# Optimization experiments

Hardware: AMD Instinct MI355X
Metric: run time of the kernel (lower is better)

## Reference

```python
import jax, jax.numpy as jnp
import numpy as np

N = 50000       # nodes
E = 800000      # edges (avg degree 16)
D = 64          # input_dim
G = 512         # graphs in batch
HID = 64        # hidden_dim


def setup_inputs() -> dict:
    key = jax.random.key(0)
    ks = jax.random.split(key, 8)
    x = jax.random.normal(ks[0], (N, D), dtype=jnp.float32)
    edge_index = jax.random.randint(ks[1], (2, E), 0, N, dtype=jnp.int64)
    batch = jnp.sort(jax.random.randint(ks[2], (N,), 0, G, dtype=jnp.int64))
    # glorot-ish scaled weights
    W1 = jax.random.normal(ks[3], (D, D), dtype=jnp.float32) * (1.0 / np.sqrt(D))
    b1 = jnp.zeros((D,), dtype=jnp.float32)
    W2 = jax.random.normal(ks[4], (D, 2 * D), dtype=jnp.float32) * (1.0 / np.sqrt(D))
    b2 = jnp.zeros((2 * D,), dtype=jnp.float32)
    Wfc = jax.random.normal(ks[5], (2 * D, HID), dtype=jnp.float32) * (1.0 / np.sqrt(2 * D))
    bfc = jnp.zeros((HID,), dtype=jnp.float32)
    return {"x": x, "edge_index": edge_index, "batch": batch,
            "W1": W1, "b1": b1, "W2": W2, "b2": b2, "Wfc": Wfc, "bfc": bfc}


def _gcn_edges(edge_index, n):
    # add self-loops (PyG GCNConv default) and symmetric normalization
    loop = jnp.arange(n, dtype=edge_index.dtype)
    src = jnp.concatenate([edge_index[0], loop])
    dst = jnp.concatenate([edge_index[1], loop])
    deg = jnp.zeros((n,), jnp.float32).at[dst].add(1.0)  # in-degree incl. self-loop
    dinv = jax.lax.rsqrt(deg)                            # deg >= 1 always
    norm = dinv[src] * dinv[dst]                         # [E+N]
    return src, dst, norm


def _gcn_conv(x, src, dst, norm, W, b):
    h = x @ W                                   # transform first (N, out)
    msg = h[src] * norm[:, None]                # gather + scale (E+N, out)
    out = jnp.zeros_like(h).at[dst].add(msg)    # scatter-add at destination
    return out + b


def reference(x, edge_index, batch, W1, b1, W2, b2, Wfc, bfc):
    n = x.shape[0]
    src, dst, norm = _gcn_edges(edge_index, n)
    h = jax.nn.relu(_gcn_conv(x, src, dst, norm, W1, b1))   # [N, D]
    h = _gcn_conv(h, src, dst, norm, W2, b2)                # [N, 2D]
    # global mean pool per graph
    sums = jax.ops.segment_sum(h, batch, num_segments=G)    # [G, 2D]
    cnt = jax.ops.segment_sum(jnp.ones((n,), h.dtype), batch, num_segments=G)
    pooled = sums / jnp.maximum(cnt, 1.0)[:, None]
    # dropout is identity in eval mode
    return pooled @ Wfc + bfc                                # [G, HID]
```

## Files before the change

### kernel.cpp

```cpp
#include <hip/hip_runtime.h>
#include <hip/hip_fp16.h>

#define NN 50000
#define EE 800000
#define DD 64
#define GG 512
#define HIDD 64
#define D2 128
#define NBLK 196

__device__ inline __half2 mk2(float a, float b) {
    __half2 h; h.x = __float2half_rn(a); h.y = __float2half_rn(b); return h;
}

__global__ void k_zero(int* __restrict__ cnt_in, int* __restrict__ part) {
    int i = blockIdx.x * blockDim.x + threadIdx.x;
    if (i < NN) cnt_in[i] = 0;
    if (i < 256) part[i] = 0;
}

__global__ void k_count_rank(const int* __restrict__ dst, int* __restrict__ cnt_in,
                             int* __restrict__ rank) {
    int e = blockIdx.x * blockDim.x + threadIdx.x;
    if (e < EE) rank[e] = atomicAdd(&cnt_in[dst[e]], 1);
}

__global__ void k_partial(const int* __restrict__ cnt_in, int* __restrict__ part) {
    __shared__ int s[256];
    int t = threadIdx.x, i = blockIdx.x * 256 + t;
    s[t] = (i < NN) ? cnt_in[i] : 0;
    __syncthreads();
    for (int off = 128; off > 0; off >>= 1) {
        if (t < off) s[t] += s[t + off];
        __syncthreads();
    }
    if (t == 0) part[blockIdx.x] = s[0];
}

__global__ void k_scanp(int* __restrict__ part) {
    __shared__ int s[256];
    int t = threadIdx.x;
    int v = part[t];
    s[t] = v;
    __syncthreads();
    for (int off = 1; off < 256; off <<= 1) {
        int add = (t >= off) ? s[t - off] : 0;
        __syncthreads();
        s[t] += add;
        __syncthreads();
    }
    part[t] = s[t] - v;
}

__global__ void k_rowptr(const int* __restrict__ cnt_in, const int* __restrict__ part,
                         int* __restrict__ rowptr) {
    __shared__ int s[256];
    int t = threadIdx.x, i = blockIdx.x * 256 + t;
    int v = (i < NN) ? cnt_in[i] : 0;
    s[t] = v;
    __syncthreads();
    for (int off = 1; off < 256; off <<= 1) {
        int add = (t >= off) ? s[t - off] : 0;
        __syncthreads();
        s[t] += add;
        __syncthreads();
    }
    int excl = s[t] - v + part[blockIdx.x];
    if (i <= NN) rowptr[i] = excl;
}

__global__ void k_place(const int* __restrict__ src, const int* __restrict__ dst,
                        const int* __restrict__ rank, const int* __restrict__ rowptr,
                        int* __restrict__ csr) {
    int e = blockIdx.x * blockDim.x + threadIdx.x;
    if (e < EE)
        csr[rowptr[dst[e]] + rank[e]] = src[e];
}

__global__ __launch_bounds__(256) void k_gemm1(const float* __restrict__ x,
        const float* __restrict__ W1, const int* __restrict__ cnt_in,
        __half2* __restrict__ t1h) {
    __shared__ float As[128][68];
    __shared__ float Bs[DD][DD];
    int t = threadIdx.x;
    int row0 = blockIdx.x * 128;
    #pragma unroll
    for (int j = 0; j < 4; ++j) {
        int id = t + j * 256;
        int k = id >> 4, c4 = (id & 15) * 4;
        *(float4*)&Bs[k][c4] = *(const float4*)&W1[k * DD + c4];
    }
    #pragma unroll
    for (int j = 0; j < 8; ++j) {
        int id = t + j * 256;
        int r = id >> 4, k4 = (id & 15) * 4;
        int gr = row0 + r;
        float4 v = make_float4(0.f, 0.f, 0.f, 0.f);
        if (gr < NN) v = *(const float4*)&x[gr * DD + k4];
        *(float4*)&As[r][k4] = v;
    }
    __syncthreads();
    int rbase = (t >> 3) * 4, cbase = (t & 7) * 8;
    float4 cL0 = make_float4(0.f,0.f,0.f,0.f), cH0 = cL0;
    float4 cL1 = cL0, cH1 = cL0, cL2 = cL0, cH2 = cL0, cL3 = cL0, cH3 = cL0;
    #pragma unroll 2
    for (int k = 0; k < DD; ++k) {
        float4 bL = *(const float4*)&Bs[k][cbase];
        float4 bH = *(const float4*)&Bs[k][cbase + 4];
        float a0 = As[rbase + 0][k];
        float a1 = As[rbase + 1][k];
        float a2 = As[rbase + 2][k];
        float a3 = As[rbase + 3][k];
        cL0 += bL * a0;  cH0 += bH * a0;
        cL1 += bL * a1;  cH1 += bH * a1;
        cL2 += bL * a2;  cH2 += bH * a2;
        cL3 += bL * a3;  cH3 += bH * a3;
    }
    int h2base = (t & 7) * 4;
    int gr0 = row0 + rbase;
    #define STORE_T1(idx, CL, CH) \
        if (gr0 + idx < NN) { \
            float d = rsqrtf((float)cnt_in[gr0 + idx] + 1.0f); \
            __half2 p0 = mk2(CL.x * d, CL.y * d), p1 = mk2(CL.z * d, CL.w * d); \
            __half2 p2 = mk2(CH.x * d, CH.y * d), p3 = mk2(CH.z * d, CH.w * d); \
            uint4 pk; pk.x = *(unsigned*)&p0; pk.y = *(unsigned*)&p1; \
            pk.z = *(unsigned*)&p2; pk.w = *(unsigned*)&p3; \
            *(uint4*)(t1h + (size_t)(gr0 + idx) * 32 + h2base) = pk; }
    STORE_T1(0, cL0, cH0)
    STORE_T1(1, cL1, cH1)
    STORE_T1(2, cL2, cH2)
    STORE_T1(3, cL3, cH3)
    #undef STORE_T1
}

__global__ __launch_bounds__(256) void k_agg1(const int* __restrict__ rowptr,
        const int* __restrict__ csr, const __half2* __restrict__ t1h,
        const int* __restrict__ cnt_in, const float* __restrict__ b1,
        __half2* __restrict__ u_h) {
    int gid = blockIdx.x * blockDim.x + threadIdx.x;
    int node = gid >> 5;
    int p = threadIdx.x & 31;
    if (node >= NN) return;
    int beg = rowptr[node], end = rowptr[node + 1];
    float2 A0 = __half22float2(t1h[(size_t)node * 32 + p]);
    float2 A1 = make_float2(0.f, 0.f), A2 = A1, A3 = A1;
    int e = beg;
    for (; e + 4 <= end; e += 4) {
        int s0 = csr[e], s1 = csr[e + 1], s2 = csr[e + 2], s3 = csr[e + 3];
        float2 v0 = __half22float2(t1h[(size_t)s0 * 32 + p]);
        float2 v1 = __half22float2(t1h[(size_t)s1 * 32 + p]);
        float2 v2 = __half22float2(t1h[(size_t)s2 * 32 + p]);
        float2 v3 = __half22float2(t1h[(size_t)s3 * 32 + p]);
        A0.x += v0.x; A0.y += v0.y;
        A1.x += v1.x; A1.y += v1.y;
        A2.x += v2.x; A2.y += v2.y;
        A3.x += v3.x; A3.y += v3.y;
    }
    for (; e < end; ++e) {
        float2 v = __half22float2(t1h[(size_t)csr[e] * 32 + p]);
        A0.x += v.x; A0.y += v.y;
    }
    float sx = (A0.x + A1.x) + (A2.x + A3.x);
    float sy = (A0.y + A1.y) + (A2.y + A3.y);
    float d = rsqrtf((float)cnt_in[node] + 1.0f);
    float2 bb = ((const float2*)b1)[p];
    float h0 = fmaxf(d * sx + bb.x, 0.0f);
    float h1 = fmaxf(d * sy + bb.y, 0.0f);
    u_h[(size_t)node * 32 + p] = mk2(d * h0, d * h1);
}

__global__ __launch_bounds__(256) void k_agg2(const int* __restrict__ rowptr,
        const int* __restrict__ csr, const __half2* __restrict__ u_h,
        const int* __restrict__ cnt_in, float* __restrict__ w) {
    int gid = blockIdx.x * blockDim.x + threadIdx.x;
    int node = gid >> 5;
    int p = threadIdx.x & 31;
    if (node >= NN) return;
    int beg = rowptr[node], end = rowptr[node + 1];
    float2 A0 = __half22float2(u_h[(size_t)node * 32 + p]);
    float2 A1 = make_float2(0.f, 0.f), A2 = A1, A3 = A1;
    int e = beg;
    for (; e + 4 <= end; e += 4) {
        int s0 = csr[e], s1 = csr[e + 1], s2 = csr[e + 2], s3 = csr[e + 3];
        float2 v0 = __half22float2(u_h[(size_t)s0 * 32 + p]);
        float2 v1 = __half22float2(u_h[(size_t)s1 * 32 + p]);
        float2 v2 = __half22float2(u_h[(size_t)s2 * 32 + p]);
        float2 v3 = __half22float2(u_h[(size_t)s3 * 32 + p]);
        A0.x += v0.x; A0.y += v0.y;
        A1.x += v1.x; A1.y += v1.y;
        A2.x += v2.x; A2.y += v2.y;
        A3.x += v3.x; A3.y += v3.y;
    }
    for (; e < end; ++e) {
        float2 v = __half22float2(u_h[(size_t)csr[e] * 32 + p]);
        A0.x += v.x; A0.y += v.y;
    }
    float d = rsqrtf((float)cnt_in[node] + 1.0f);
    float sx = (A0.x + A1.x) + (A2.x + A3.x);
    float sy = (A0.y + A1.y) + (A2.y + A3.y);
    ((float2*)&w[(size_t)node * DD])[p] = make_float2(d * sx, d * sy);
}

__global__ __launch_bounds__(128) void k_pool2(const float* __restrict__ w,
        const int* __restrict__ batch, const float* __restrict__ W2,
        const float* __restrict__ b2, const float* __restrict__ Wfc,
        const float* __restrict__ bfc, float* __restrict__ out) {
    int g = blockIdx.x;
    int t = threadIdx.x;
    int c = t & 63, half = t >> 6;
    int lo = 0, hi = NN;
    while (lo < hi) { int mid = (lo + hi) >> 1; if (batch[mid] < g) lo = mid + 1; else hi = mid; }
    int beg = lo;
    hi = NN;
    while (lo < hi) { int mid = (lo + hi) >> 1; if (batch[mid] < g + 1) lo = mid + 1; else hi = mid; }
    int end = lo;
    int n = end - beg;

    float s = 0.0f;
    for (int i = beg + half; i < end; i += 2)
        s += w[(size_t)i * DD + c];

    __shared__ float sm[128];
    __shared__ float pm[DD];
    __shared__ float tt[D2];
    sm[t] = s;
    __syncthreads();
    if (t < DD) {
        float scale = (n > 0) ? (1.0f / (float)n) : 0.0f;
        pm[t] = (sm[t] + sm[t + 64]) * scale;
    }
    __syncthreads();
    {
        float acc = (n > 0) ? b2[t] : 0.0f;
        #pragma unroll 4
        for (int k = 0; k < DD; ++k)
            acc += pm[k] * W2[k * D2 + t];
        tt[t] = acc;
    }
    __syncthreads();
    if (t < HIDD) {
        float o = bfc[t];
        #pragma unroll 4
        for (int k = 0; k < D2; ++k)
            o += tt[k] * Wfc[k * HIDD + t];
        out[g * HIDD + t] = o;
    }
}

extern "C" void kernel_launch(void* const* d_in, const int* in_sizes, int n_in,
                              void* d_out, int out_size, void* d_ws, size_t ws_size,
                              hipStream_t stream) {
    const float* x     = (const float*)d_in[0];
    const int*   ei    = (const int*)  d_in[1];
    const int*   batch = (const int*)  d_in[2];
    const float* W1    = (const float*)d_in[3];
    const float* b1    = (const float*)d_in[4];
    const float* W2    = (const float*)d_in[5];
    const float* b2    = (const float*)d_in[6];
    const float* Wfc   = (const float*)d_in[7];
    const float* bfc   = (const float*)d_in[8];
    float* out = (float*)d_out;

    const int* src = ei;
    const int* dst = ei + EE;

    char* base = (char*)d_ws;
    __half2* t1h  = (__half2*)base;
    __half2* u_h  = (__half2*)(base + (size_t)NN * 128);
    float*   w    = (float*)(base + (size_t)NN * 512);
    int* iws    = (int*)(base + (size_t)NN * 512 + (size_t)NN * 256);
    int* cnt_in = iws;
    int* rowptr = cnt_in + 50048;
    int* part   = rowptr + 50304;
    int* rank   = part + 256;
    int* csr    = rank + EE;

    k_zero      <<<NBLK, 256, 0, stream>>>(cnt_in, part);
    k_count_rank<<<(EE + 255) / 256, 256, 0, stream>>>(dst, cnt_in, rank);
    k_partial   <<<NBLK, 256, 0, stream>>>(cnt_in, part);
    k_scanp     <<<1, 256, 0, stream>>>(part);
    k_rowptr    <<<NBLK, 256, 0, stream>>>(cnt_in, part, rowptr);
    k_place     <<<(EE + 255) / 256, 256, 0, stream>>>(src, dst, rank, rowptr, csr);
    k_gemm1     <<<(NN + 127) / 128, 256, 0, stream>>>(x, W1, cnt_in, t1h);
    k_agg1      <<<(NN * 32 + 255) / 256, 256, 0, stream>>>(rowptr, csr, t1h, cnt_in, b1, u_h);
    k_agg2      <<<(NN * 32 + 255) / 256, 256, 0, stream>>>(rowptr, csr, u_h, cnt_in, w);
    k_pool2     <<<GG, 128, 0, stream>>>(w, batch, W2, b2, Wfc, bfc, out);
}
```

Baseline: 219.8 us.

## Fuse second aggregation into per-graph pooling and merge scan kernels

The second neighbor aggregation now runs inside the per-graph pooling kernel: each block handles one graph, its warps aggregate that graph's nodes and reduce them in shared memory. This removes the intermediate w buffer write and read and one launch. The three-kernel row-pointer scan is replaced by one kernel where each block recomputes its prefix by summing all preceding counts. That removes launches but adds redundant reads, and the fused pool kernel has less parallelism and can be imbalanced across graphs.

```diff
diff --git a/kernel.cpp b/kernel.cpp
--- a/kernel.cpp
+++ b/kernel.cpp
@@ -13,10 +13,9 @@
     __half2 h; h.x = __float2half_rn(a); h.y = __float2half_rn(b); return h;
 }
 
-__global__ void k_zero(int* __restrict__ cnt_in, int* __restrict__ part) {
+__global__ void k_zero(int* __restrict__ cnt_in) {
     int i = blockIdx.x * blockDim.x + threadIdx.x;
     if (i < NN) cnt_in[i] = 0;
-    if (i < 256) part[i] = 0;
 }
 
 __global__ void k_count_rank(const int* __restrict__ dst, int* __restrict__ cnt_in,
@@ -25,22 +24,24 @@
     if (e < EE) rank[e] = atomicAdd(&cnt_in[dst[e]], 1);
 }
 
-__global__ void k_partial(const int* __restrict__ cnt_in, int* __restrict__ part) {
+__global__ __launch_bounds__(256) void k_scan_rowptr(const int* __restrict__ cnt_in,
+                                                     int* __restrict__ rowptr) {
+    int b = blockIdx.x, t = threadIdx.x;
+    int base = b * 256;
+    int prior = 0;
+    for (int i = t; i < base; i += 256) prior += cnt_in[i];
+    __shared__ int red[256];
+    red[t] = prior;
+    __syncthreads();
+    for (int off = 128; off > 0; off >>= 1) {
+        if (t < off) red[t] += red[t + off];
+        __syncthreads();
+    }
+    int blockPrefix = red[0];
+    __syncthreads();
+    int i = base + t;
+    int v = (i < NN) ? cnt_in[i] : 0;
     __shared__ int s[256];
-    int t = threadIdx.x, i = blockIdx.x * 256 + t;
-    s[t] = (i < NN) ? cnt_in[i] : 0;
-    __syncthreads();
-    for (int off = 128; off > 0; off >>= 1) {
-        if (t < off) s[t] += s[t + off];
-        __syncthreads();
-    }
-    if (t == 0) part[blockIdx.x] = s[0];
-}
-
-__global__ void k_scanp(int* __restrict__ part) {
-    __shared__ int s[256];
-    int t = threadIdx.x;
-    int v = part[t];
     s[t] = v;
     __syncthreads();
     for (int off = 1; off < 256; off <<= 1) {
@@ -49,24 +50,7 @@
         s[t] += add;
         __syncthreads();
     }
-    part[t] = s[t] - v;
-}
-
-__global__ void k_rowptr(const int* __restrict__ cnt_in, const int* __restrict__ part,
-                         int* __restrict__ rowptr) {
-    __shared__ int s[256];
-    int t = threadIdx.x, i = blockIdx.x * 256 + t;
-    int v = (i < NN) ? cnt_in[i] : 0;
-    s[t] = v;
-    __syncthreads();
-    for (int off = 1; off < 256; off <<= 1) {
-        int add = (t >= off) ? s[t - off] : 0;
-        __syncthreads();
-        s[t] += add;
-        __syncthreads();
-    }
-    int excl = s[t] - v + part[blockIdx.x];
-    if (i <= NN) rowptr[i] = excl;
+    if (i <= NN) rowptr[i] = s[t] - v + blockPrefix;
 }
 
 __global__ void k_place(const int* __restrict__ src, const int* __restrict__ dst,
@@ -169,45 +153,15 @@
     u_h[(size_t)node * 32 + p] = mk2(d * h0, d * h1);
 }
 
-__global__ __launch_bounds__(256) void k_agg2(const int* __restrict__ rowptr,
+__global__ __launch_bounds__(256) void k_pool3(const int* __restrict__ rowptr,
         const int* __restrict__ csr, const __half2* __restrict__ u_h,
-        const int* __restrict__ cnt_in, float* __restrict__ w) {
-    int gid = blockIdx.x * blockDim.x + threadIdx.x;
-    int node = gid >> 5;
-    int p = threadIdx.x & 31;
-    if (node >= NN) return;
-    int beg = rowptr[node], end = rowptr[node + 1];
-    float2 A0 = __half22float2(u_h[(size_t)node * 32 + p]);
-    float2 A1 = make_float2(0.f, 0.f), A2 = A1, A3 = A1;
-    int e = beg;
-    for (; e + 4 <= end; e += 4) {
-        int s0 = csr[e], s1 = csr[e + 1], s2 = csr[e + 2], s3 = csr[e + 3];
-        float2 v0 = __half22float2(u_h[(size_t)s0 * 32 + p]);
-        float2 v1 = __half22float2(u_h[(size_t)s1 * 32 + p]);
-        float2 v2 = __half22float2(u_h[(size_t)s2 * 32 + p]);
-        float2 v3 = __half22float2(u_h[(size_t)s3 * 32 + p]);
-        A0.x += v0.x; A0.y += v0.y;
-        A1.x += v1.x; A1.y += v1.y;
-        A2.x += v2.x; A2.y += v2.y;
-        A3.x += v3.x; A3.y += v3.y;
-    }
-    for (; e < end; ++e) {
-        float2 v = __half22float2(u_h[(size_t)csr[e] * 32 + p]);
-        A0.x += v.x; A0.y += v.y;
-    }
-    float d = rsqrtf((float)cnt_in[node] + 1.0f);
-    float sx = (A0.x + A1.x) + (A2.x + A3.x);
-    float sy = (A0.y + A1.y) + (A2.y + A3.y);
-    ((float2*)&w[(size_t)node * DD])[p] = make_float2(d * sx, d * sy);
-}
-
-__global__ __launch_bounds__(128) void k_pool2(const float* __restrict__ w,
-        const int* __restrict__ batch, const float* __restrict__ W2,
-        const float* __restrict__ b2, const float* __restrict__ Wfc,
-        const float* __restrict__ bfc, float* __restrict__ out) {
+        const int* __restrict__ cnt_in, const int* __restrict__ batch,
+        const float* __restrict__ W2, const float* __restrict__ b2,
+        const float* __restrict__ Wfc, const float* __restrict__ bfc,
+        float* __restrict__ out) {
     int g = blockIdx.x;
     int t = threadIdx.x;
-    int c = t & 63, half = t >> 6;
+    int sw = t >> 5, p = t & 31;
     int lo = 0, hi = NN;
     while (lo < hi) { int mid = (lo + hi) >> 1; if (batch[mid] < g) lo = mid + 1; else hi = mid; }
     int beg = lo;
@@ -216,21 +170,46 @@
     int end = lo;
     int n = end - beg;
 
-    float s = 0.0f;
-    for (int i = beg + half; i < end; i += 2)
-        s += w[(size_t)i * DD + c];
-
-    __shared__ float sm[128];
+    float2 gacc = make_float2(0.f, 0.f);
+    for (int node = beg + sw; node < end; node += 8) {
+        int nb = rowptr[node], ne = rowptr[node + 1];
+        float2 A0 = __half22float2(u_h[(size_t)node * 32 + p]);
+        float2 A1 = make_float2(0.f, 0.f), A2 = A1, A3 = A1;
+        int e = nb;
+        for (; e + 4 <= ne; e += 4) {
+            int s0 = csr[e], s1 = csr[e + 1], s2 = csr[e + 2], s3 = csr[e + 3];
+            float2 v0 = __half22float2(u_h[(size_t)s0 * 32 + p]);
+            float2 v1 = __half22float2(u_h[(size_t)s1 * 32 + p]);
+            float2 v2 = __half22float2(u_h[(size_t)s2 * 32 + p]);
+            float2 v3 = __half22float2(u_h[(size_t)s3 * 32 + p]);
+            A0.x += v0.x; A0.y += v0.y;
+            A1.x += v1.x; A1.y += v1.y;
+            A2.x += v2.x; A2.y += v2.y;
+            A3.x += v3.x; A3.y += v3.y;
+        }
+        for (; e < ne; ++e) {
+            float2 v = __half22float2(u_h[(size_t)csr[e] * 32 + p]);
+            A0.x += v.x; A0.y += v.y;
+        }
+        float d = rsqrtf((float)cnt_in[node] + 1.0f);
+        gacc.x += d * ((A0.x + A1.x) + (A2.x + A3.x));
+        gacc.y += d * ((A0.y + A1.y) + (A2.y + A3.y));
+    }
+    __shared__ float2 red[32][9];
+    red[p][sw] = gacc;
+    __syncthreads();
     __shared__ float pm[DD];
+    if (t < 32) {
+        float2 s = red[t][0];
+        #pragma unroll
+        for (int j = 1; j < 8; ++j) { s.x += red[t][j].x; s.y += red[t][j].y; }
+        float scale = (n > 0) ? (1.0f / (float)n) : 0.0f;
+        pm[2 * t]     = s.x * scale;
+        pm[2 * t + 1] = s.y * scale;
+    }
+    __syncthreads();
     __shared__ float tt[D2];
-    sm[t] = s;
-    __syncthreads();
-    if (t < DD) {
-        float scale = (n > 0) ? (1.0f / (float)n) : 0.0f;
-        pm[t] = (sm[t] + sm[t + 64]) * scale;
-    }
-    __syncthreads();
-    {
+    if (t < D2) {
         float acc = (n > 0) ? b2[t] : 0.0f;
         #pragma unroll 4
         for (int k = 0; k < DD; ++k)
@@ -265,24 +244,19 @@
     const int* dst = ei + EE;
 
     char* base = (char*)d_ws;
-    __half2* t1h  = (__half2*)base;
-    __half2* u_h  = (__half2*)(base + (size_t)NN * 128);
-    float*   w    = (float*)(base + (size_t)NN * 512);
-    int* iws    = (int*)(base + (size_t)NN * 512 + (size_t)NN * 256);
+    __half2* t1h = (__half2*)base;
+    __half2* u_h = (__half2*)(base + (size_t)NN * 128);
+    int* iws    = (int*)(base + (size_t)NN * 256);
     int* cnt_in = iws;
     int* rowptr = cnt_in + 50048;
-    int* part   = rowptr + 50304;
-    int* rank   = part + 256;
+    int* rank   = rowptr + 50304;
     int* csr    = rank + EE;
 
-    k_zero      <<<NBLK, 256, 0, stream>>>(cnt_in, part);
-    k_count_rank<<<(EE + 255) / 256, 256, 0, stream>>>(dst, cnt_in, rank);
-    k_partial   <<<NBLK, 256, 0, stream>>>(cnt_in, part);
-    k_scanp     <<<1, 256, 0, stream>>>(part);
-    k_rowptr    <<<NBLK, 256, 0, stream>>>(cnt_in, part, rowptr);
-    k_place     <<<(EE + 255) / 256, 256, 0, stream>>>(src, dst, rank, rowptr, csr);
-    k_gemm1     <<<(NN + 127) / 128, 256, 0, stream>>>(x, W1, cnt_in, t1h);
-    k_agg1      <<<(NN * 32 + 255) / 256, 256, 0, stream>>>(rowptr, csr, t1h, cnt_in, b1, u_h);
-    k_agg2      <<<(NN * 32 + 255) / 256, 256, 0, stream>>>(rowptr, csr, u_h, cnt_in, w);
-    k_pool2     <<<GG, 128, 0, stream>>>(w, batch, W2, b2, Wfc, bfc, out);
-}
+    k_zero       <<<NBLK, 256, 0, stream>>>(cnt_in);
+    k_count_rank <<<(EE + 255) / 256, 256, 0, stream>>>(dst, cnt_in, rank);
+    k_scan_rowptr<<<NBLK, 256, 0, stream>>>(cnt_in, rowptr);
+    k_place      <<<(EE + 255) / 256, 256, 0, stream>>>(src, dst, rank, rowptr, csr);
+    k_gemm1      <<<(NN + 127) / 128, 256, 0, stream>>>(x, W1, cnt_in, t1h);
+    k_agg1       <<<(NN * 32 + 255) / 256, 256, 0, stream>>>(rowptr, csr, t1h, cnt_in, b1, u_h);
+    k_pool3      <<<GG, 256, 0, stream>>>(rowptr, csr, u_h, cnt_in, batch, W2, b2, Wfc, bfc, out);
+}
```

After: 263.8 us. 1.2x slower.
